# Kernel optimization log

Hardware: AMD Instinct MI355X
Metric: run time of the kernel (lower is better)

## Reference

```python
import jax, jax.numpy as jnp
import numpy as np

N = 131072          # batch_size(64) * cycle_size(2048) total graph nodes
E = 2097152         # N * avg_degree(16) edges


def _gcn_block(x, edge_index, W_self, W_nbr, b):
    """GraphConv-style STGCN spatial block: self-transform + mean-aggregated
    neighbor transform over edge_index (gather -> segment-reduce -> scatter)."""
    src, dst = edge_index[0], edge_index[1]
    msg = jax.ops.segment_sum(x[src], dst, num_segments=N)            # [N, C_in]
    deg = jax.ops.segment_sum(jnp.ones((edge_index.shape[1],), x.dtype), dst,
                              num_segments=N)                          # [N]
    agg = msg / jnp.maximum(deg, 1.0)[:, None]
    return x @ W_self + agg @ W_nbr + b


def setup_inputs() -> dict:
    key = jax.random.key(0)
    ks = jax.random.split(key, 16)

    def lin(k, fan_in, fan_out):
        return jax.random.normal(k, (fan_in, fan_out), jnp.float32) / np.sqrt(fan_in)

    x = jax.random.normal(ks[0], (N, 16), jnp.float32)
    edge_index = jax.random.randint(ks[1], (2, E), 0, N)
    batch = jnp.zeros((N,), jnp.int64) if jax.config.jax_enable_x64 else jnp.zeros((N,), jnp.int32)

    return {
        "x": x,
        "edge_index": edge_index,
        "batch": batch,
        "W_lin": lin(ks[2], 16, 16),
        "b_lin": jnp.zeros((16,), jnp.float32),
        # block3: 16 -> 32
        "Ws3": lin(ks[3], 16, 32), "Wn3": lin(ks[4], 16, 32), "b3": jnp.zeros((32,), jnp.float32),
        # block2: 32 -> 64
        "Ws2": lin(ks[5], 32, 64), "Wn2": lin(ks[6], 32, 64), "b2": jnp.zeros((64,), jnp.float32),
        # block1: 64 -> 128
        "Ws1": lin(ks[7], 64, 128), "Wn1": lin(ks[8], 64, 128), "b1": jnp.zeros((128,), jnp.float32),
    }


def reference(x, edge_index, batch, W_lin, b_lin,
              Ws3, Wn3, b3, Ws2, Wn2, b2, Ws1, Wn1, b1):
    h = x @ W_lin + b_lin                                   # Linear(16,16)
    h = jax.nn.relu(_gcn_block(h, edge_index, Ws3, Wn3, b3))   # 16 -> 32
    h = jax.nn.relu(_gcn_block(h, edge_index, Ws2, Wn2, b2))   # 32 -> 64
    h = jax.nn.sigmoid(_gcn_block(h, edge_index, Ws1, Wn1, b1))  # 64 -> 128
    return h
```

## Files before the change

### kernel.cpp

```cpp
#include <hip/hip_runtime.h>
#include <cmath>


typedef __attribute__((ext_vector_type(8))) _Float16 half8;
typedef __attribute__((ext_vector_type(4))) float floatx4;

#define NBUCKET 512
#define BUCKET_SHIFT 8

__global__ __launch_bounds__(256) void bucket_hist_kernel(
    const int* __restrict__ dst, int* __restrict__ bcnt, int E, int EPB, int nblk) {
    __shared__ int lh[NBUCKET];
    for (int i = threadIdx.x; i < NBUCKET; i += 256) lh[i] = 0;
    __syncthreads();
    int base = blockIdx.x * EPB;
    int end  = min(base + EPB, E);
    for (int i = base + threadIdx.x; i < end; i += 256)
        atomicAdd(&lh[dst[i] >> BUCKET_SHIFT], 1);
    __syncthreads();
    for (int i = threadIdx.x; i < NBUCKET; i += 256)
        bcnt[i * nblk + blockIdx.x] = lh[i];
}

__global__ void scan1_kernel(const int* __restrict__ in, int* __restrict__ out,
                             int* __restrict__ bsum) {
    __shared__ int s[256];
    int i = blockIdx.x * 256 + threadIdx.x;
    int v = in[i];
    s[threadIdx.x] = v;
    __syncthreads();
    for (int off = 1; off < 256; off <<= 1) {
        int t = (threadIdx.x >= off) ? s[threadIdx.x - off] : 0;
        __syncthreads();
        s[threadIdx.x] += t;
        __syncthreads();
    }
    out[i] = s[threadIdx.x] - v;
    if (threadIdx.x == 255) bsum[blockIdx.x] = s[255];
}

__global__ void scan2_kernel(int* __restrict__ bsum, int NB) {
    extern __shared__ int s2[];
    int v = (threadIdx.x < NB) ? bsum[threadIdx.x] : 0;
    s2[threadIdx.x] = v;
    __syncthreads();
    for (int off = 1; off < NB; off <<= 1) {
        int t = (threadIdx.x >= off) ? s2[threadIdx.x - off] : 0;
        __syncthreads();
        s2[threadIdx.x] += t;
        __syncthreads();
    }
    if (threadIdx.x < NB) bsum[threadIdx.x] = s2[threadIdx.x] - v;
}

__global__ void scan3_kernel(int* __restrict__ out, const int* __restrict__ bsum) {
    int i = blockIdx.x * 256 + threadIdx.x;
    out[i] += bsum[blockIdx.x];
}

__global__ __launch_bounds__(256) void partition_kernel(
    const int* __restrict__ src, const int* __restrict__ dst,
    const int* __restrict__ bofs, int2* __restrict__ part,
    int E, int EPB, int nblk) {
    __shared__ int cur[NBUCKET];
    for (int i = threadIdx.x; i < NBUCKET; i += 256)
        cur[i] = bofs[i * nblk + blockIdx.x];
    __syncthreads();
    int base = blockIdx.x * EPB;
    int end  = min(base + EPB, E);
    for (int i = base + threadIdx.x; i < end; i += 256) {
        int d = dst[i];
        int p = atomicAdd(&cur[d >> BUCKET_SHIFT], 1);
        part[p] = make_int2(src[i], d);
    }
}

__global__ __launch_bounds__(256) void local_csr_kernel(
    const int* __restrict__ bofs, const int2* __restrict__ part,
    int* __restrict__ row_ptr, int* __restrict__ csr_src,
    int N, int E, int nblk) {
    __shared__ int cnt[256];
    __shared__ int offs[256];
    const int u      = blockIdx.x;
    const int node0  = u << BUCKET_SHIFT;
    const int bstart = bofs[(size_t)u * nblk];
    const int bend   = (u + 1 < gridDim.x) ? bofs[(size_t)(u + 1) * nblk] : E;

    cnt[threadIdx.x] = 0;
    __syncthreads();
    for (int i = bstart + threadIdx.x; i < bend; i += 256)
        atomicAdd(&cnt[part[i].y - node0], 1);
    __syncthreads();

    int v = cnt[threadIdx.x];
    offs[threadIdx.x] = v;
    __syncthreads();
    for (int off = 1; off < 256; off <<= 1) {
        int t = (threadIdx.x >= off) ? offs[threadIdx.x - off] : 0;
        __syncthreads();
        offs[threadIdx.x] += t;
        __syncthreads();
    }
    int excl = offs[threadIdx.x] - v;
    int rbase = bstart + excl;
    if (node0 + threadIdx.x < N) row_ptr[node0 + threadIdx.x] = rbase;
    if (u == 0 && threadIdx.x == 0) row_ptr[N] = E;
    __syncthreads();
    cnt[threadIdx.x] = rbase;
    __syncthreads();
    for (int i = bstart + threadIdx.x; i < bend; i += 256) {
        int2 e = part[i];
        int p = atomicAdd(&cnt[e.y - node0], 1);
        csr_src[p] = e.x;
    }
}

__global__ void wt_kernel(const float* __restrict__ Ws, const float* __restrict__ Wn,
                          _Float16* __restrict__ Wt, int CI, int NOUT) {
    int K = 2 * CI;
    int idx = blockIdx.x * 256 + threadIdx.x;
    if (idx >= NOUT * K) return;
    int n = idx / K, k = idx - n * K;
    float v = (k < CI) ? Ws[(size_t)k * NOUT + n] : Wn[(size_t)(k - CI) * NOUT + n];
    Wt[idx] = (_Float16)v;
}

__global__ void lin16_kernel(const float* __restrict__ x, const float* __restrict__ W,
                             const float* __restrict__ b, _Float16* __restrict__ h, int N) {
    __shared__ float sW[256];
    __shared__ float sb[16];
    sW[threadIdx.x] = W[threadIdx.x];
    if (threadIdx.x < 16) sb[threadIdx.x] = b[threadIdx.x];
    __syncthreads();
    int n = blockIdx.x * blockDim.x + threadIdx.x;
    if (n >= N) return;
    const float4* xr = (const float4*)(x + (size_t)n * 16);
    float4 x0 = xr[0], x1 = xr[1], x2 = xr[2], x3 = xr[3];
    float xi[16] = {x0.x, x0.y, x0.z, x0.w, x1.x, x1.y, x1.z, x1.w,
                    x2.x, x2.y, x2.z, x2.w, x3.x, x3.y, x3.z, x3.w};
    float o[16];
#pragma unroll
    for (int j = 0; j < 16; j++) o[j] = sb[j];
#pragma unroll
    for (int k = 0; k < 16; k++) {
        float xv = xi[k];
#pragma unroll
        for (int j = 0; j < 16; j++) o[j] += xv * sW[k * 16 + j];
    }
    half8 h0v, h1v;
#pragma unroll
    for (int j = 0; j < 8; j++) { h0v[j] = (_Float16)o[j]; h1v[j] = (_Float16)o[j + 8]; }
    half8* hr = (half8*)(h + (size_t)n * 16);
    hr[0] = h0v;
    hr[1] = h1v;
}

template <int C>
__global__ __launch_bounds__(256) void gather_kernel(
    const int* __restrict__ row_ptr, const int* __restrict__ csr_src,
    const _Float16* __restrict__ h, _Float16* __restrict__ agg, int N) {
    constexpr int GP = C / 8;
    int t = blockIdx.x * blockDim.x + threadIdx.x;
    int total = N * GP;
    if (t >= total) return;
    int n = t / GP;
    int g = t - n * GP;
    const int beg = row_ptr[n];
    const int end = row_ptr[n + 1];
    const size_t goff = (size_t)g * 8;

    float a0[8], a1[8];
#pragma unroll
    for (int i = 0; i < 8; i++) { a0[i] = 0.f; a1[i] = 0.f; }

    int j = beg;
    for (; j + 8 <= end; j += 8) {
        int i0 = csr_src[j + 0], i1 = csr_src[j + 1], i2 = csr_src[j + 2], i3 = csr_src[j + 3];
        int i4 = csr_src[j + 4], i5 = csr_src[j + 5], i6 = csr_src[j + 6], i7 = csr_src[j + 7];
        half8 v0 = *(const half8*)(h + (size_t)i0 * C + goff);
        half8 v1 = *(const half8*)(h + (size_t)i1 * C + goff);
        half8 v2 = *(const half8*)(h + (size_t)i2 * C + goff);
        half8 v3 = *(const half8*)(h + (size_t)i3 * C + goff);
        half8 v4 = *(const half8*)(h + (size_t)i4 * C + goff);
        half8 v5 = *(const half8*)(h + (size_t)i5 * C + goff);
        half8 v6 = *(const half8*)(h + (size_t)i6 * C + goff);
        half8 v7 = *(const half8*)(h + (size_t)i7 * C + goff);
#pragma unroll
        for (int i = 0; i < 8; i++) {
            a0[i] += ((float)v0[i] + (float)v2[i]) + ((float)v4[i] + (float)v6[i]);
            a1[i] += ((float)v1[i] + (float)v3[i]) + ((float)v5[i] + (float)v7[i]);
        }
    }
    if (j < end) {
        const int last = end - 1;
        int i0 = csr_src[j];
        int i1 = csr_src[min(j + 1, last)];
        int i2 = csr_src[min(j + 2, last)];
        int i3 = csr_src[min(j + 3, last)];
        int i4 = csr_src[min(j + 4, last)];
        int i5 = csr_src[min(j + 5, last)];
        int i6 = csr_src[min(j + 6, last)];
        int i7 = csr_src[min(j + 7, last)];
        half8 v0 = *(const half8*)(h + (size_t)i0 * C + goff);
        half8 v1 = *(const half8*)(h + (size_t)i1 * C + goff);
        half8 v2 = *(const half8*)(h + (size_t)i2 * C + goff);
        half8 v3 = *(const half8*)(h + (size_t)i3 * C + goff);
        half8 v4 = *(const half8*)(h + (size_t)i4 * C + goff);
        half8 v5 = *(const half8*)(h + (size_t)i5 * C + goff);
        half8 v6 = *(const half8*)(h + (size_t)i6 * C + goff);
        half8 v7 = *(const half8*)(h + (size_t)i7 * C + goff);
        float w1 = (j + 1 < end) ? 1.f : 0.f;
        float w2 = (j + 2 < end) ? 1.f : 0.f;
        float w3 = (j + 3 < end) ? 1.f : 0.f;
        float w4 = (j + 4 < end) ? 1.f : 0.f;
        float w5 = (j + 5 < end) ? 1.f : 0.f;
        float w6 = (j + 6 < end) ? 1.f : 0.f;
        float w7 = (j + 7 < end) ? 1.f : 0.f;
#pragma unroll
        for (int i = 0; i < 8; i++) {
            a0[i] += ((float)v0[i] + w2 * (float)v2[i]) + (w4 * (float)v4[i] + w6 * (float)v6[i]);
            a1[i] += (w1 * (float)v1[i] + w3 * (float)v3[i]) + (w5 * (float)v5[i] + w7 * (float)v7[i]);
        }
    }

    float inv = 1.0f / fmaxf((float)(end - beg), 1.0f);
    half8 r;
#pragma unroll
    for (int i = 0; i < 8; i++) r[i] = (_Float16)((a0[i] + a1[i]) * inv);
    *(half8*)(agg + (size_t)n * C + goff) = r;
}

template <int CI, int NOUT, int ACT, bool OUT_F16>
__global__ __launch_bounds__(256) void mfma_gemm_kernel(
    const _Float16* __restrict__ hbuf, const _Float16* __restrict__ abuf,
    const _Float16* __restrict__ Wt,
    const float* __restrict__ bias, void* __restrict__ outp, int N)
{
    constexpr int K   = 2 * CI;
    constexpr int KS  = K / 32;
    constexpr int CT  = NOUT / 16;
    constexpr int LDW = K + 8;
    __shared__ _Float16 Bt[NOUT * LDW];

    const int tid = threadIdx.x;
    for (int idx = tid; idx < NOUT * (K / 8); idx += 256) {
        int n  = idx / (K / 8);
        int kq = idx - n * (K / 8);
        *(half8*)&Bt[n * LDW + kq * 8] = *(const half8*)(Wt + (size_t)n * K + kq * 8);
    }
    __syncthreads();

    const int wave = tid >> 6;
    const int lane = tid & 63;
    const int m    = lane & 15;
    const int quad = lane >> 4;
    const int row0 = blockIdx.x * 64 + wave * 16;
    const size_t row = (size_t)(row0 + m);

    floatx4 acc[CT];
#pragma unroll
    for (int c = 0; c < CT; c++) acc[c] = (floatx4){0.f, 0.f, 0.f, 0.f};

#pragma unroll
    for (int s = 0; s < KS; s++) {
        int k8 = s * 32 + quad * 8;
        const _Float16* Ap = (k8 < CI) ? (hbuf + row * CI + k8)
                                       : (abuf + row * CI + (k8 - CI));
        half8 a = *(const half8*)Ap;
#pragma unroll
        for (int c = 0; c < CT; c++) {
            half8 b = *(const half8*)&Bt[(c * 16 + m) * LDW + k8];
            acc[c] = __builtin_amdgcn_mfma_f32_16x16x32_f16(a, b, acc[c], 0, 0, 0);
        }
    }

#pragma unroll
    for (int c = 0; c < CT; c++) {
        int col = c * 16 + m;
        float bv = bias[col];
#pragma unroll
        for (int j = 0; j < 4; j++) {
            int orow = row0 + quad * 4 + j;
            float v = acc[c][j] + bv;
            if (ACT == 0) v = fmaxf(v, 0.0f);
            else          v = 1.0f / (1.0f + __expf(-v));
            if (OUT_F16) ((_Float16*)outp)[(size_t)orow * NOUT + col] = (_Float16)v;
            else         ((float*)outp)[(size_t)orow * NOUT + col] = v;
        }
    }
}

extern "C" void kernel_launch(void* const* d_in, const int* in_sizes, int n_in,
                              void* d_out, int out_size, void* d_ws, size_t ws_size,
                              hipStream_t stream) {
    const float* x     = (const float*)d_in[0];
    const int*   ei    = (const int*)d_in[1];
    const float* W_lin = (const float*)d_in[3];
    const float* b_lin = (const float*)d_in[4];
    const float* Ws3   = (const float*)d_in[5];
    const float* Wn3   = (const float*)d_in[6];
    const float* b3    = (const float*)d_in[7];
    const float* Ws2   = (const float*)d_in[8];
    const float* Wn2   = (const float*)d_in[9];
    const float* b2    = (const float*)d_in[10];
    const float* Ws1   = (const float*)d_in[11];
    const float* Wn1   = (const float*)d_in[12];
    const float* b1    = (const float*)d_in[13];
    float* out = (float*)d_out;

    const int N = in_sizes[0] / 16;
    const int E = in_sizes[1] / 2;
    const int* src = ei;
    const int* dst = ei + E;

    const int NBLK = 512;
    const int EPB  = (E + NBLK - 1) / NBLK;
    const int M    = NBUCKET * NBLK;
    const int NB2  = M / 256;

    int* wsi = (int*)d_ws;
    int* row_ptr = wsi;
    size_t B0 = ((size_t)(N + 1) + 3) & ~(size_t)3;
    int* bcnt = wsi + B0;
    int* bofs = bcnt + M;
    int* bsum = bofs + M;
    size_t C0 = (B0 + 2 * (size_t)M + (size_t)NB2 + 3) & ~(size_t)3;
    int* csr_src = wsi + C0;
    size_t P0 = (C0 + (size_t)E + 3) & ~(size_t)3;
    int2* part = (int2*)(wsi + P0);
    size_t H0 = (P0 + 2 * (size_t)E + 3) & ~(size_t)3;
    _Float16* regA = (_Float16*)(wsi + H0);
    _Float16* regB = regA + (size_t)64 * N;
    _Float16* Wt1  = regB + (size_t)64 * N;
    _Float16* Wt2  = Wt1 + 16384;
    _Float16* Wt3  = Wt2 + 4096;

    _Float16* h0    = regA;
    _Float16* agg16 = regA + (size_t)16 * N;
    _Float16* h2    = regA;
    _Float16* h3    = regB;
    _Float16* agg32 = regB + (size_t)32 * N;
    _Float16* agg64 = regB;

    const int BLK = 256;

    wt_kernel<<<(32 * 32 + 255) / 256, 256, 0, stream>>>(Ws3, Wn3, Wt3, 16, 32);
    wt_kernel<<<(64 * 64 + 255) / 256, 256, 0, stream>>>(Ws2, Wn2, Wt2, 32, 64);
    wt_kernel<<<(128 * 128 + 255) / 256, 256, 0, stream>>>(Ws1, Wn1, Wt1, 64, 128);

    bucket_hist_kernel<<<NBLK, 256, 0, stream>>>(dst, bcnt, E, EPB, NBLK);
    scan1_kernel<<<NB2, 256, 0, stream>>>(bcnt, bofs, bsum);
    scan2_kernel<<<1, NB2, NB2 * sizeof(int), stream>>>(bsum, NB2);
    scan3_kernel<<<NB2, 256, 0, stream>>>(bofs, bsum);
    partition_kernel<<<NBLK, 256, 0, stream>>>(src, dst, bofs, part, E, EPB, NBLK);
    local_csr_kernel<<<NBUCKET, 256, 0, stream>>>(bofs, part, row_ptr, csr_src, N, E, NBLK);

    lin16_kernel<<<(N + BLK - 1) / BLK, BLK, 0, stream>>>(x, W_lin, b_lin, h0, N);

    gather_kernel<16><<<((size_t)N * 2 + BLK - 1) / BLK, BLK, 0, stream>>>(row_ptr, csr_src, h0, agg16, N);
    mfma_gemm_kernel<16, 32, 0, true><<<N / 64, 256, 0, stream>>>(h0, agg16, Wt3, b3, h3, N);

    gather_kernel<32><<<((size_t)N * 4 + BLK - 1) / BLK, BLK, 0, stream>>>(row_ptr, csr_src, h3, agg32, N);
    mfma_gemm_kernel<32, 64, 0, true><<<N / 64, 256, 0, stream>>>(h3, agg32, Wt2, b2, h2, N);

    gather_kernel<64><<<((size_t)N * 8 + BLK - 1) / BLK, BLK, 0, stream>>>(row_ptr, csr_src, h2, agg64, N);
    mfma_gemm_kernel<64, 128, 1, false><<<N / 64, 256, 0, stream>>>(h2, agg64, Wt1, b1, out, N);
}
```

Baseline: 336.7 us.

## Store features in 16-channel slabs and gather each slab separately

Intermediate f16 feature maps move from row-major [N,C] to a channel-slab layout [C/16][N][16], and the GEMM reads and writes that layout. Each wider gather becomes several launches of a single 16-channel gather kernel, one per slab, so every random gather touches a 32-byte row whose working set (N*16 halves, 4 MB) can stay cache-resident. The cost is re-reading row_ptr/csr_src once per slab and issuing more kernel launches. Index loads and the output store also become nontemporal.

```diff
diff --git a/kernel.cpp b/kernel.cpp
--- a/kernel.cpp
+++ b/kernel.cpp
@@ -155,16 +155,13 @@
     hr[1] = h1v;
 }
 
-template <int C>
-__global__ __launch_bounds__(256) void gather_kernel(
+__global__ __launch_bounds__(256) void gather16_kernel(
     const int* __restrict__ row_ptr, const int* __restrict__ csr_src,
     const _Float16* __restrict__ h, _Float16* __restrict__ agg, int N) {
-    constexpr int GP = C / 8;
-    int t = blockIdx.x * blockDim.x + threadIdx.x;
-    int total = N * GP;
-    if (t >= total) return;
-    int n = t / GP;
-    int g = t - n * GP;
+    int t = blockIdx.x * 256 + threadIdx.x;
+    if (t >= N * 2) return;
+    int n = t >> 1;
+    int g = t & 1;
     const int beg = row_ptr[n];
     const int end = row_ptr[n + 1];
     const size_t goff = (size_t)g * 8;
@@ -175,16 +172,22 @@
 
     int j = beg;
     for (; j + 8 <= end; j += 8) {
-        int i0 = csr_src[j + 0], i1 = csr_src[j + 1], i2 = csr_src[j + 2], i3 = csr_src[j + 3];
-        int i4 = csr_src[j + 4], i5 = csr_src[j + 5], i6 = csr_src[j + 6], i7 = csr_src[j + 7];
-        half8 v0 = *(const half8*)(h + (size_t)i0 * C + goff);
-        half8 v1 = *(const half8*)(h + (size_t)i1 * C + goff);
-        half8 v2 = *(const half8*)(h + (size_t)i2 * C + goff);
-        half8 v3 = *(const half8*)(h + (size_t)i3 * C + goff);
-        half8 v4 = *(const half8*)(h + (size_t)i4 * C + goff);
-        half8 v5 = *(const half8*)(h + (size_t)i5 * C + goff);
-        half8 v6 = *(const half8*)(h + (size_t)i6 * C + goff);
-        half8 v7 = *(const half8*)(h + (size_t)i7 * C + goff);
+        int i0 = __builtin_nontemporal_load(csr_src + j + 0);
+        int i1 = __builtin_nontemporal_load(csr_src + j + 1);
+        int i2 = __builtin_nontemporal_load(csr_src + j + 2);
+        int i3 = __builtin_nontemporal_load(csr_src + j + 3);
+        int i4 = __builtin_nontemporal_load(csr_src + j + 4);
+        int i5 = __builtin_nontemporal_load(csr_src + j + 5);
+        int i6 = __builtin_nontemporal_load(csr_src + j + 6);
+        int i7 = __builtin_nontemporal_load(csr_src + j + 7);
+        half8 v0 = *(const half8*)(h + (size_t)i0 * 16 + goff);
+        half8 v1 = *(const half8*)(h + (size_t)i1 * 16 + goff);
+        half8 v2 = *(const half8*)(h + (size_t)i2 * 16 + goff);
+        half8 v3 = *(const half8*)(h + (size_t)i3 * 16 + goff);
+        half8 v4 = *(const half8*)(h + (size_t)i4 * 16 + goff);
+        half8 v5 = *(const half8*)(h + (size_t)i5 * 16 + goff);
+        half8 v6 = *(const half8*)(h + (size_t)i6 * 16 + goff);
+        half8 v7 = *(const half8*)(h + (size_t)i7 * 16 + goff);
 #pragma unroll
         for (int i = 0; i < 8; i++) {
             a0[i] += ((float)v0[i] + (float)v2[i]) + ((float)v4[i] + (float)v6[i]);
@@ -201,14 +204,14 @@
         int i5 = csr_src[min(j + 5, last)];
         int i6 = csr_src[min(j + 6, last)];
         int i7 = csr_src[min(j + 7, last)];
-        half8 v0 = *(const half8*)(h + (size_t)i0 * C + goff);
-        half8 v1 = *(const half8*)(h + (size_t)i1 * C + goff);
-        half8 v2 = *(const half8*)(h + (size_t)i2 * C + goff);
-        half8 v3 = *(const half8*)(h + (size_t)i3 * C + goff);
-        half8 v4 = *(const half8*)(h + (size_t)i4 * C + goff);
-        half8 v5 = *(const half8*)(h + (size_t)i5 * C + goff);
-        half8 v6 = *(const half8*)(h + (size_t)i6 * C + goff);
-        half8 v7 = *(const half8*)(h + (size_t)i7 * C + goff);
+        half8 v0 = *(const half8*)(h + (size_t)i0 * 16 + goff);
+        half8 v1 = *(const half8*)(h + (size_t)i1 * 16 + goff);
+        half8 v2 = *(const half8*)(h + (size_t)i2 * 16 + goff);
+        half8 v3 = *(const half8*)(h + (size_t)i3 * 16 + goff);
+        half8 v4 = *(const half8*)(h + (size_t)i4 * 16 + goff);
+        half8 v5 = *(const half8*)(h + (size_t)i5 * 16 + goff);
+        half8 v6 = *(const half8*)(h + (size_t)i6 * 16 + goff);
+        half8 v7 = *(const half8*)(h + (size_t)i7 * 16 + goff);
         float w1 = (j + 1 < end) ? 1.f : 0.f;
         float w2 = (j + 2 < end) ? 1.f : 0.f;
         float w3 = (j + 3 < end) ? 1.f : 0.f;
@@ -227,7 +230,7 @@
     half8 r;
 #pragma unroll
     for (int i = 0; i < 8; i++) r[i] = (_Float16)((a0[i] + a1[i]) * inv);
-    *(half8*)(agg + (size_t)n * C + goff) = r;
+    __builtin_nontemporal_store(r, (half8*)(agg + (size_t)n * 16 + goff));
 }
 
 template <int CI, int NOUT, int ACT, bool OUT_F16>
@@ -264,8 +267,9 @@
 #pragma unroll
     for (int s = 0; s < KS; s++) {
         int k8 = s * 32 + quad * 8;
-        const _Float16* Ap = (k8 < CI) ? (hbuf + row * CI + k8)
-                                       : (abuf + row * CI + (k8 - CI));
+        int kk = (k8 < CI) ? k8 : k8 - CI;
+        const _Float16* base = (k8 < CI) ? hbuf : abuf;
+        const _Float16* Ap = base + ((size_t)(kk >> 4)) * N * 16 + row * 16 + (kk & 15);
         half8 a = *(const half8*)Ap;
 #pragma unroll
         for (int c = 0; c < CT; c++) {
@@ -284,8 +288,10 @@
             float v = acc[c][j] + bv;
             if (ACT == 0) v = fmaxf(v, 0.0f);
             else          v = 1.0f / (1.0f + __expf(-v));
-            if (OUT_F16) ((_Float16*)outp)[(size_t)orow * NOUT + col] = (_Float16)v;
-            else         ((float*)outp)[(size_t)orow * NOUT + col] = v;
+            if (OUT_F16)
+                ((_Float16*)outp)[(size_t)c * N * 16 + (size_t)orow * 16 + m] = (_Float16)v;
+            else
+                ((float*)outp)[(size_t)orow * NOUT + col] = v;
         }
     }
 }
@@ -343,6 +349,7 @@
     _Float16* agg64 = regB;
 
     const int BLK = 256;
+    const int GGRID = (2 * N + BLK - 1) / BLK;
 
     wt_kernel<<<(32 * 32 + 255) / 256, 256, 0, stream>>>(Ws3, Wn3, Wt3, 16, 32);
     wt_kernel<<<(64 * 64 + 255) / 256, 256, 0, stream>>>(Ws2, Wn2, Wt2, 32, 64);
@@ -357,12 +364,16 @@
 
     lin16_kernel<<<(N + BLK - 1) / BLK, BLK, 0, stream>>>(x, W_lin, b_lin, h0, N);
 
-    gather_kernel<16><<<((size_t)N * 2 + BLK - 1) / BLK, BLK, 0, stream>>>(row_ptr, csr_src, h0, agg16, N);
+    gather16_kernel<<<GGRID, BLK, 0, stream>>>(row_ptr, csr_src, h0, agg16, N);
     mfma_gemm_kernel<16, 32, 0, true><<<N / 64, 256, 0, stream>>>(h0, agg16, Wt3, b3, h3, N);
 
-    gather_kernel<32><<<((size_t)N * 4 + BLK - 1) / BLK, BLK, 0, stream>>>(row_ptr, csr_src, h3, agg32, N);
+    for (int c = 0; c < 2; c++)
+        gather16_kernel<<<GGRID, BLK, 0, stream>>>(
+            row_ptr, csr_src, h3 + (size_t)c * N * 16, agg32 + (size_t)c * N * 16, N);
     mfma_gemm_kernel<32, 64, 0, true><<<N / 64, 256, 0, stream>>>(h3, agg32, Wt2, b2, h2, N);
 
-    gather_kernel<64><<<((size_t)N * 8 + BLK - 1) / BLK, BLK, 0, stream>>>(row_ptr, csr_src, h2, agg64, N);
+    for (int c = 0; c < 4; c++)
+        gather16_kernel<<<GGRID, BLK, 0, stream>>>(
+            row_ptr, csr_src, h2 + (size_t)c * N * 16, agg64 + (size_t)c * N * 16, N);
     mfma_gemm_kernel<64, 128, 1, false><<<N / 64, 256, 0, stream>>>(h2, agg64, Wt1, b1, out, N);
 }
```

After: 379.4 us. +12.7%, slower.

## Pack partition entries into one int, merge weight prep kernels, halve partition blocks

Applied to the files above, without the earlier changes.

The partition buffer now stores each edge as a single 32-bit word, the source index shifted left by 8 with the low 8 bits of the destination, instead of an int2. This halves the partition write and read traffic in the CSR build. The three weight-transpose launches are merged into one kernel, and the number of partition blocks drops from 512 to 256, which also shrinks the histogram and scan work. The packing only works while source indices fit in 24 bits, so it limits the supported node count.

```diff
diff --git a/kernel.cpp b/kernel.cpp
--- a/kernel.cpp
+++ b/kernel.cpp
@@ -60,7 +60,7 @@
 
 __global__ __launch_bounds__(256) void partition_kernel(
     const int* __restrict__ src, const int* __restrict__ dst,
-    const int* __restrict__ bofs, int2* __restrict__ part,
+    const int* __restrict__ bofs, int* __restrict__ part,
     int E, int EPB, int nblk) {
     __shared__ int cur[NBUCKET];
     for (int i = threadIdx.x; i < NBUCKET; i += 256)
@@ -71,12 +71,12 @@
     for (int i = base + threadIdx.x; i < end; i += 256) {
         int d = dst[i];
         int p = atomicAdd(&cur[d >> BUCKET_SHIFT], 1);
-        part[p] = make_int2(src[i], d);
+        part[p] = (src[i] << 8) | (d & 255);
     }
 }
 
 __global__ __launch_bounds__(256) void local_csr_kernel(
-    const int* __restrict__ bofs, const int2* __restrict__ part,
+    const int* __restrict__ bofs, const int* __restrict__ part,
     int* __restrict__ row_ptr, int* __restrict__ csr_src,
     int N, int E, int nblk) {
     __shared__ int cnt[256];
@@ -89,7 +89,7 @@
     cnt[threadIdx.x] = 0;
     __syncthreads();
     for (int i = bstart + threadIdx.x; i < bend; i += 256)
-        atomicAdd(&cnt[part[i].y - node0], 1);
+        atomicAdd(&cnt[part[i] & 255], 1);
     __syncthreads();
 
     int v = cnt[threadIdx.x];
@@ -109,20 +109,26 @@
     cnt[threadIdx.x] = rbase;
     __syncthreads();
     for (int i = bstart + threadIdx.x; i < bend; i += 256) {
-        int2 e = part[i];
-        int p = atomicAdd(&cnt[e.y - node0], 1);
-        csr_src[p] = e.x;
-    }
-}
-
-__global__ void wt_kernel(const float* __restrict__ Ws, const float* __restrict__ Wn,
-                          _Float16* __restrict__ Wt, int CI, int NOUT) {
+        int e = part[i];
+        int p = atomicAdd(&cnt[e & 255], 1);
+        csr_src[p] = e >> 8;
+    }
+}
+
+__global__ void wt_all_kernel(
+    const float* __restrict__ Ws1, const float* __restrict__ Wn1, _Float16* __restrict__ Wt1,
+    const float* __restrict__ Ws2, const float* __restrict__ Wn2, _Float16* __restrict__ Wt2,
+    const float* __restrict__ Ws3, const float* __restrict__ Wn3, _Float16* __restrict__ Wt3) {
+    int idx = blockIdx.x * 256 + threadIdx.x;
+    const float *Ws, *Wn; _Float16* Wt; int CI, NOUT;
+    if (idx < 16384)        { Ws = Ws1; Wn = Wn1; Wt = Wt1; CI = 64; NOUT = 128; }
+    else if (idx < 20480)   { idx -= 16384; Ws = Ws2; Wn = Wn2; Wt = Wt2; CI = 32; NOUT = 64; }
+    else if (idx < 21504)   { idx -= 20480; Ws = Ws3; Wn = Wn3; Wt = Wt3; CI = 16; NOUT = 32; }
+    else return;
     int K = 2 * CI;
-    int idx = blockIdx.x * 256 + threadIdx.x;
-    if (idx >= NOUT * K) return;
     int n = idx / K, k = idx - n * K;
     float v = (k < CI) ? Ws[(size_t)k * NOUT + n] : Wn[(size_t)(k - CI) * NOUT + n];
-    Wt[idx] = (_Float16)v;
+    Wt[n * K + k] = (_Float16)v;
 }
 
 __global__ void lin16_kernel(const float* __restrict__ x, const float* __restrict__ W,
@@ -313,7 +319,7 @@
     const int* src = ei;
     const int* dst = ei + E;
 
-    const int NBLK = 512;
+    const int NBLK = 256;
     const int EPB  = (E + NBLK - 1) / NBLK;
     const int M    = NBUCKET * NBLK;
     const int NB2  = M / 256;
@@ -327,8 +333,8 @@
     size_t C0 = (B0 + 2 * (size_t)M + (size_t)NB2 + 3) & ~(size_t)3;
     int* csr_src = wsi + C0;
     size_t P0 = (C0 + (size_t)E + 3) & ~(size_t)3;
-    int2* part = (int2*)(wsi + P0);
-    size_t H0 = (P0 + 2 * (size_t)E + 3) & ~(size_t)3;
+    int* part = wsi + P0;
+    size_t H0 = (P0 + (size_t)E + 3) & ~(size_t)3;
     _Float16* regA = (_Float16*)(wsi + H0);
     _Float16* regB = regA + (size_t)64 * N;
     _Float16* Wt1  = regB + (size_t)64 * N;
@@ -344,9 +350,8 @@
 
     const int BLK = 256;
 
-    wt_kernel<<<(32 * 32 + 255) / 256, 256, 0, stream>>>(Ws3, Wn3, Wt3, 16, 32);
-    wt_kernel<<<(64 * 64 + 255) / 256, 256, 0, stream>>>(Ws2, Wn2, Wt2, 32, 64);
-    wt_kernel<<<(128 * 128 + 255) / 256, 256, 0, stream>>>(Ws1, Wn1, Wt1, 64, 128);
+    wt_all_kernel<<<(21504 + 255) / 256, 256, 0, stream>>>(
+        Ws1, Wn1, Wt1, Ws2, Wn2, Wt2, Ws3, Wn3, Wt3);
 
     bucket_hist_kernel<<<NBLK, 256, 0, stream>>>(dst, bcnt, E, EPB, NBLK);
     scan1_kernel<<<NB2, 256, 0, stream>>>(bcnt, bofs, bsum);
```

New measurement: 325.0 us, median of 2. 3.5% less time.
